# Kernel tuning notes

Measured on AMD Instinct MI355X. Metric: run time of the kernel, lower is better.

## Reference

```python
import jax, jax.numpy as jnp
import numpy as np

ALPHA = 0.7
MARGIN = 0.5
BATCH = 8192


def setup_inputs() -> dict:
    key = jax.random.key(0)
    k1, k2 = jax.random.split(key)
    predictions = jax.random.normal(k1, (BATCH, 1), dtype=jnp.float32)
    targets = jax.random.normal(k2, (BATCH, 1), dtype=jnp.float32)
    return {"predictions": predictions, "targets": targets}


def reference(predictions, targets):
    # MSE term (mean over all elements, as nn.MSELoss default)
    mse_loss = jnp.mean((predictions - targets) ** 2)

    p = predictions[:, 0]  # [B]
    t = targets[:, 0]      # [B]
    B = p.shape[0]

    # Pairwise differences [B, B]
    dt = t[:, None] - t[None, :]
    dp = p[:, None] - p[None, :]

    # Original loop visits ordered pairs i < j and, depending on sign(t_i - t_j),
    # computes relu(margin - sign(t_i - t_j) * (p_i - p_j)); ties are skipped.
    upper = jnp.triu(jnp.ones((B, B), dtype=bool), k=1)
    valid = upper & (dt != 0)
    pair_loss = jax.nn.relu(MARGIN - jnp.sign(dt) * dp)

    count = jnp.sum(valid)
    ranking_sum = jnp.sum(jnp.where(valid, pair_loss, 0.0))
    ranking_loss = jnp.where(count > 0, ranking_sum / jnp.maximum(count, 1), 0.0)

    return ALPHA * mse_loss + (1.0 - ALPHA) * ranking_loss
```

## Files before the change

### kernel.cpp

```cpp
#include <hip/hip_runtime.h>

#define ALPHA 0.7f
#define MARGIN 0.5f
#define TI 128
#define TJ 256

__global__ __launch_bounds__(256) void pair_kernel(const float* __restrict__ p,
                                                   const float* __restrict__ t,
                                                   int B,
                                                   float* __restrict__ bsum,
                                                   float* __restrict__ bmse,
                                                   int*   __restrict__ bcnt) {
    const int bid = blockIdx.x;
    int jt = (int)((sqrtf(4.0f * (float)bid + 1.0f) - 1.0f) * 0.5f);
    while ((jt + 1) * (jt + 2) <= bid) ++jt;
    while (jt * (jt + 1) > bid) --jt;
    const int it = bid - jt * (jt + 1);

    const int tid = threadIdx.x;
    const int ig0 = it * TI;
    const int jg  = jt * TJ + tid;

    __shared__ float s_t[TI];
    __shared__ float s_p[TI];
    if (tid < TI) {
        const int ig = ig0 + tid;
        const bool iv = ig < B;
        s_t[tid] = iv ? t[ig] : 0.0f;
        s_p[tid] = iv ? p[ig] : 0.0f;
    }
    __syncthreads();

    const bool jvalid = jg < B;
    const float tjv = jvalid ? t[jg] : 0.0f;
    const float pjv = jvalid ? p[jg] : 0.0f;

    float sum  = 0.0f;
    int   cnt  = 0;
    float msev = 0.0f;

    const bool fulltile = (ig0 + TI) <= jt * TJ;

    if (jvalid) {
        if (it == 2 * jt) {
            const float d = pjv - tjv;
            msev = d * d;
        }
        if (fulltile) {
            #pragma unroll 8
            for (int ii = 0; ii < TI; ++ii) {
                const float dt = s_t[ii] - tjv;
                const float dp = s_p[ii] - pjv;
                const float sdp = (dt > 0.0f) ? dp : -dp;
                const float v = fmaxf(MARGIN - sdp, 0.0f);
                const bool valid = (dt != 0.0f);
                sum += valid ? v : 0.0f;
                cnt += valid ? 1 : 0;
            }
        } else {
            const int ilim = min(TI, B - ig0);
            const int jloc = jg - ig0;
            #pragma unroll 4
            for (int ii = 0; ii < ilim; ++ii) {
                const float dt = s_t[ii] - tjv;
                const float dp = s_p[ii] - pjv;
                const float sdp = (dt > 0.0f) ? dp : -dp;
                const float v = fmaxf(MARGIN - sdp, 0.0f);
                const bool valid = (dt != 0.0f) && (ii < jloc);
                sum += valid ? v : 0.0f;
                cnt += valid ? 1 : 0;
            }
        }
    }

    for (int off = 32; off > 0; off >>= 1) {
        sum  += __shfl_down(sum, off);
        cnt  += __shfl_down(cnt, off);
        msev += __shfl_down(msev, off);
    }
    __shared__ float r_sum[4], r_mse[4];
    __shared__ int   r_cnt[4];
    const int wid  = tid >> 6;
    const int lane = tid & 63;
    if (lane == 0) { r_sum[wid] = sum; r_mse[wid] = msev; r_cnt[wid] = cnt; }
    __syncthreads();
    if (tid == 0) {
        bsum[bid] = r_sum[0] + r_sum[1] + r_sum[2] + r_sum[3];
        bmse[bid] = r_mse[0] + r_mse[1] + r_mse[2] + r_mse[3];
        bcnt[bid] = r_cnt[0] + r_cnt[1] + r_cnt[2] + r_cnt[3];
    }
}

__global__ __launch_bounds__(256) void finalize_kernel(const float* __restrict__ bsum,
                                                       const float* __restrict__ bmse,
                                                       const int*   __restrict__ bcnt,
                                                       int NB, int B,
                                                       float* __restrict__ out) {
    const int tid = threadIdx.x;
    double S = 0.0, M = 0.0;
    long long C = 0;
    for (int k = tid; k < NB; k += 256) {
        S += (double)bsum[k];
        M += (double)bmse[k];
        C += (long long)bcnt[k];
    }
    for (int off = 32; off > 0; off >>= 1) {
        S += __shfl_down(S, off);
        M += __shfl_down(M, off);
        C += __shfl_down(C, off);
    }
    __shared__ double rs[4], rm[4];
    __shared__ long long rc[4];
    const int wid  = tid >> 6;
    const int lane = tid & 63;
    if (lane == 0) { rs[wid] = S; rm[wid] = M; rc[wid] = C; }
    __syncthreads();
    if (tid == 0) {
        S = rs[0] + rs[1] + rs[2] + rs[3];
        M = rm[0] + rm[1] + rm[2] + rm[3];
        C = rc[0] + rc[1] + rc[2] + rc[3];
        const double mse  = M / (double)B;
        const double rank = (C > 0) ? (S / (double)(C > 1 ? C : 1)) : 0.0;
        out[0] = (float)((double)ALPHA * mse + (double)(1.0f - ALPHA) * rank);
    }
}

extern "C" void kernel_launch(void* const* d_in, const int* in_sizes, int n_in,
                              void* d_out, int out_size, void* d_ws, size_t ws_size,
                              hipStream_t stream) {
    const float* p = (const float*)d_in[0];
    const float* t = (const float*)d_in[1];
    const int B = in_sizes[0];

    const int NJ = (B + TJ - 1) / TJ;
    const int NB = NJ * (NJ + 1);

    float* bsum = (float*)d_ws;
    float* bmse = bsum + NB;
    int*   bcnt = (int*)(bmse + NB);

    pair_kernel<<<NB, TJ, 0, stream>>>(p, t, B, bsum, bmse, bcnt);
    finalize_kernel<<<1, 256, 0, stream>>>(bsum, bmse, bcnt, NB, B, (float*)d_out);
}
```

Baseline: 19.85 us.

## Register-block four j columns per thread with single-wave blocks and ballot counts

Each thread now handles four j columns in registers and loads them with float4 reads. Blocks shrink to one 64-lane wave, so the i-tile is 64 rows, and the triangular block mapping is redone for the finer tiles. Shared memory stores t and p as interleaved float2. The sign flip uses a bit XOR, and the valid-pair count uses ballot plus popcount instead of per-thread integer adds. The block-level shared reduction is dropped. The trade-off is more blocks, each with less work, and extra ballot instructions in the inner loop.

After: 22.50 us. 13.3% more time.

```diff
diff --git a/kernel.cpp b/kernel.cpp
--- a/kernel.cpp
+++ b/kernel.cpp
@@ -1,93 +1,119 @@
 #include <hip/hip_runtime.h>
 
-#define ALPHA 0.7f
+#define ALPHA  0.7f
 #define MARGIN 0.5f
-#define TI 128
+#define TI 64
 #define TJ 256
+#define JR 4
 
-__global__ __launch_bounds__(256) void pair_kernel(const float* __restrict__ p,
-                                                   const float* __restrict__ t,
-                                                   int B,
-                                                   float* __restrict__ bsum,
-                                                   float* __restrict__ bmse,
-                                                   int*   __restrict__ bcnt) {
+__global__ __launch_bounds__(64) void pair_kernel(const float* __restrict__ p,
+                                                  const float* __restrict__ t,
+                                                  int B,
+                                                  float* __restrict__ bsum,
+                                                  float* __restrict__ bmse,
+                                                  int*   __restrict__ bcnt) {
     const int bid = blockIdx.x;
-    int jt = (int)((sqrtf(4.0f * (float)bid + 1.0f) - 1.0f) * 0.5f);
-    while ((jt + 1) * (jt + 2) <= bid) ++jt;
-    while (jt * (jt + 1) > bid) --jt;
-    const int it = bid - jt * (jt + 1);
+    int jt = (int)((sqrtf(1.0f + 2.0f * (float)bid) - 1.0f) * 0.5f);
+    while (2 * (jt + 1) * (jt + 2) <= bid) ++jt;
+    while (2 * jt * (jt + 1) > bid) --jt;
+    const int it  = bid - 2 * jt * (jt + 1);
 
-    const int tid = threadIdx.x;
-    const int ig0 = it * TI;
-    const int jg  = jt * TJ + tid;
+    const int tid   = threadIdx.x;
+    const int ig0   = it * TI;
+    const int jbase = jt * TJ;
+    const int j0    = jbase + tid * JR;
 
-    __shared__ float s_t[TI];
-    __shared__ float s_p[TI];
-    if (tid < TI) {
+    __shared__ float2 s_tp[TI];
+    {
         const int ig = ig0 + tid;
-        const bool iv = ig < B;
-        s_t[tid] = iv ? t[ig] : 0.0f;
-        s_p[tid] = iv ? p[ig] : 0.0f;
+        float2 v;
+        if (ig < B) { v.x = t[ig]; v.y = p[ig]; }
+        else        { v.x = 0.0f;  v.y = 0.0f;  }
+        s_tp[tid] = v;
     }
     __syncthreads();
 
-    const bool jvalid = jg < B;
-    const float tjv = jvalid ? t[jg] : 0.0f;
-    const float pjv = jvalid ? p[jg] : 0.0f;
+    float tjv[JR], pjv[JR];
+    bool  jvb[JR];
+    if (j0 + JR <= B) {
+        const float4 tv = *reinterpret_cast<const float4*>(t + j0);
+        const float4 pv = *reinterpret_cast<const float4*>(p + j0);
+        tjv[0] = tv.x; tjv[1] = tv.y; tjv[2] = tv.z; tjv[3] = tv.w;
+        pjv[0] = pv.x; pjv[1] = pv.y; pjv[2] = pv.z; pjv[3] = pv.w;
+        jvb[0] = jvb[1] = jvb[2] = jvb[3] = true;
+    } else {
+        #pragma unroll
+        for (int k = 0; k < JR; ++k) {
+            const int jg = j0 + k;
+            jvb[k] = jg < B;
+            tjv[k] = jvb[k] ? t[jg] : 0.0f;
+            pjv[k] = jvb[k] ? p[jg] : 0.0f;
+        }
+    }
+    unsigned long long jm[JR];
+    #pragma unroll
+    for (int k = 0; k < JR; ++k) jm[k] = __ballot(jvb[k]);
 
-    float sum  = 0.0f;
-    int   cnt  = 0;
+    float sum[JR] = {0.0f, 0.0f, 0.0f, 0.0f};
+    int   cnt = 0;
     float msev = 0.0f;
 
-    const bool fulltile = (ig0 + TI) <= jt * TJ;
+    if (it == 4 * jt) {
+        #pragma unroll
+        for (int k = 0; k < JR; ++k) {
+            const float d = pjv[k] - tjv[k];
+            msev += jvb[k] ? d * d : 0.0f;
+        }
+    }
 
-    if (jvalid) {
-        if (it == 2 * jt) {
-            const float d = pjv - tjv;
-            msev = d * d;
+    if (it < 4 * jt) {
+        #pragma unroll 8
+        for (int ii = 0; ii < TI; ++ii) {
+            const float2 itp = s_tp[ii];
+            #pragma unroll
+            for (int k = 0; k < JR; ++k) {
+                const float dt = itp.x - tjv[k];
+                const float dp = itp.y - pjv[k];
+                const unsigned sg = __float_as_uint(dt) & 0x80000000u;
+                const float sdp = __uint_as_float(__float_as_uint(dp) ^ sg);
+                const float v = fmaxf(MARGIN - sdp, 0.0f);
+                const bool val = (dt != 0.0f);
+                sum[k] += val ? v : 0.0f;
+                cnt += (int)__popcll(__ballot(val) & jm[k]);
+            }
         }
-        if (fulltile) {
-            #pragma unroll 8
-            for (int ii = 0; ii < TI; ++ii) {
-                const float dt = s_t[ii] - tjv;
-                const float dp = s_p[ii] - pjv;
-                const float sdp = (dt > 0.0f) ? dp : -dp;
+    } else {
+        int jloc[JR];
+        #pragma unroll
+        for (int k = 0; k < JR; ++k) jloc[k] = j0 + k - ig0;
+        #pragma unroll 4
+        for (int ii = 0; ii < TI; ++ii) {
+            const float2 itp = s_tp[ii];
+            #pragma unroll
+            for (int k = 0; k < JR; ++k) {
+                const float dt = itp.x - tjv[k];
+                const float dp = itp.y - pjv[k];
+                const unsigned sg = __float_as_uint(dt) & 0x80000000u;
+                const float sdp = __uint_as_float(__float_as_uint(dp) ^ sg);
                 const float v = fmaxf(MARGIN - sdp, 0.0f);
-                const bool valid = (dt != 0.0f);
-                sum += valid ? v : 0.0f;
-                cnt += valid ? 1 : 0;
-            }
-        } else {
-            const int ilim = min(TI, B - ig0);
-            const int jloc = jg - ig0;
-            #pragma unroll 4
-            for (int ii = 0; ii < ilim; ++ii) {
-                const float dt = s_t[ii] - tjv;
-                const float dp = s_p[ii] - pjv;
-                const float sdp = (dt > 0.0f) ? dp : -dp;
-                const float v = fmaxf(MARGIN - sdp, 0.0f);
-                const bool valid = (dt != 0.0f) && (ii < jloc);
-                sum += valid ? v : 0.0f;
-                cnt += valid ? 1 : 0;
+                const bool val = (dt != 0.0f) && (ii < jloc[k]);
+                sum[k] += val ? v : 0.0f;
+                cnt += (int)__popcll(__ballot(val) & jm[k]);
             }
         }
     }
 
+    float stot = 0.0f;
+    #pragma unroll
+    for (int k = 0; k < JR; ++k) stot += jvb[k] ? sum[k] : 0.0f;
     for (int off = 32; off > 0; off >>= 1) {
-        sum  += __shfl_down(sum, off);
-        cnt  += __shfl_down(cnt, off);
+        stot += __shfl_down(stot, off);
         msev += __shfl_down(msev, off);
     }
-    __shared__ float r_sum[4], r_mse[4];
-    __shared__ int   r_cnt[4];
-    const int wid  = tid >> 6;
-    const int lane = tid & 63;
-    if (lane == 0) { r_sum[wid] = sum; r_mse[wid] = msev; r_cnt[wid] = cnt; }
-    __syncthreads();
     if (tid == 0) {
-        bsum[bid] = r_sum[0] + r_sum[1] + r_sum[2] + r_sum[3];
-        bmse[bid] = r_mse[0] + r_mse[1] + r_mse[2] + r_mse[3];
-        bcnt[bid] = r_cnt[0] + r_cnt[1] + r_cnt[2] + r_cnt[3];
+        bsum[bid] = stot;
+        bmse[bid] = msev;
+        bcnt[bid] = cnt;
     }
 }
 
@@ -111,8 +137,7 @@
     }
     __shared__ double rs[4], rm[4];
     __shared__ long long rc[4];
-    const int wid  = tid >> 6;
-    const int lane = tid & 63;
+    const int wid = tid >> 6, lane = tid & 63;
     if (lane == 0) { rs[wid] = S; rm[wid] = M; rc[wid] = C; }
     __syncthreads();
     if (tid == 0) {
@@ -133,12 +158,12 @@
     const int B = in_sizes[0];
 
     const int NJ = (B + TJ - 1) / TJ;
-    const int NB = NJ * (NJ + 1);
+    const int NB = 2 * NJ * (NJ + 1);
 
     float* bsum = (float*)d_ws;
     float* bmse = bsum + NB;
     int*   bcnt = (int*)(bmse + NB);
 
-    pair_kernel<<<NB, TJ, 0, stream>>>(p, t, B, bsum, bmse, bcnt);
+    pair_kernel<<<NB, 64, 0, stream>>>(p, t, B, bsum, bmse, bcnt);
     finalize_kernel<<<1, 256, 0, stream>>>(bsum, bmse, bcnt, NB, B, (float*)d_out);
 }
```

## Retile pair kernel with two j per thread and deferred tie handling

Applied to the files above, without the earlier changes.

Changes the tiling to 64-row i tiles by 512-column j tiles, with each thread handling two j elements loaded as float2. The i values now come straight from global memory as uniform loads instead of through shared memory. The sign flip becomes a bitwise XOR, and the tie check moves to a rare wave-uniform branch so the main loop is branch-free. The pair count is worked out in closed form minus the ties, and 4 blocks per SM are requested through launch bounds. The aim is fewer shared-memory and sync costs and more ILP per thread, at the price of more blocks and partials for the finalize kernel and reliance on scalar-cache hits for the i loads.

Measured after the change: 21.08 us. 6.2% more time.

```diff
diff --git a/kernel.cpp b/kernel.cpp
--- a/kernel.cpp
+++ b/kernel.cpp
@@ -1,93 +1,127 @@
 #include <hip/hip_runtime.h>
 
-#define ALPHA 0.7f
+#define ALPHA  0.7f
 #define MARGIN 0.5f
-#define TI 128
-#define TJ 256
+#define TI  64
+#define TJ  512
+#define JR  2
 
-__global__ __launch_bounds__(256) void pair_kernel(const float* __restrict__ p,
-                                                   const float* __restrict__ t,
-                                                   int B,
-                                                   float* __restrict__ bsum,
-                                                   float* __restrict__ bmse,
-                                                   int*   __restrict__ bcnt) {
+__global__ __launch_bounds__(256, 4)
+void pair_kernel(const float* __restrict__ p, const float* __restrict__ t,
+                 int B, float* __restrict__ bsum, float* __restrict__ bmse,
+                 int* __restrict__ bcnt) {
     const int bid = blockIdx.x;
-    int jt = (int)((sqrtf(4.0f * (float)bid + 1.0f) - 1.0f) * 0.5f);
-    while ((jt + 1) * (jt + 2) <= bid) ++jt;
-    while (jt * (jt + 1) > bid) --jt;
-    const int it = bid - jt * (jt + 1);
+    int jt = (int)((sqrtf((float)bid + 1.0f) - 1.0f) * 0.5f);
+    while (4 * (jt + 1) * (jt + 2) <= bid) ++jt;
+    while (4 * jt * (jt + 1) > bid) --jt;
+    const int it = bid - 4 * jt * (jt + 1);
 
-    const int tid = threadIdx.x;
-    const int ig0 = it * TI;
-    const int jg  = jt * TJ + tid;
+    const int tid   = threadIdx.x;
+    const int ibase = it * TI;
+    const int j0    = jt * TJ + tid * JR;
 
-    __shared__ float s_t[TI];
-    __shared__ float s_p[TI];
-    if (tid < TI) {
-        const int ig = ig0 + tid;
-        const bool iv = ig < B;
-        s_t[tid] = iv ? t[ig] : 0.0f;
-        s_p[tid] = iv ? p[ig] : 0.0f;
+    float tjv0, tjv1, pjv0, pjv1;
+    bool jv0, jv1;
+    if (j0 + JR <= B) {
+        const float2 tv = *reinterpret_cast<const float2*>(t + j0);
+        const float2 pv = *reinterpret_cast<const float2*>(p + j0);
+        tjv0 = tv.x; tjv1 = tv.y; pjv0 = pv.x; pjv1 = pv.y;
+        jv0 = jv1 = true;
+    } else {
+        jv0 = (j0 + 0) < B;
+        jv1 = (j0 + 1) < B;
+        tjv0 = jv0 ? t[j0]     : __int_as_float(0x7f800000);
+        tjv1 = jv1 ? t[j0 + 1] : __int_as_float(0x7f800000);
+        pjv0 = jv0 ? p[j0]     : 1e30f;
+        pjv1 = jv1 ? p[j0 + 1] : 1e30f;
     }
-    __syncthreads();
 
-    const bool jvalid = jg < B;
-    const float tjv = jvalid ? t[jg] : 0.0f;
-    const float pjv = jvalid ? p[jg] : 0.0f;
+    float sum = 0.0f, msev = 0.0f;
+    int   cnt = 0, tiec = 0;
 
-    float sum  = 0.0f;
-    int   cnt  = 0;
-    float msev = 0.0f;
+    if (it == 0) {
+        const float d0 = pjv0 - tjv0, d1 = pjv1 - tjv1;
+        msev += jv0 ? d0 * d0 : 0.0f;
+        msev += jv1 ? d1 * d1 : 0.0f;
+    }
 
-    const bool fulltile = (ig0 + TI) <= jt * TJ;
+    const int ilim = min(TI, B - ibase);
 
-    if (jvalid) {
-        if (it == 2 * jt) {
-            const float d = pjv - tjv;
-            msev = d * d;
-        }
-        if (fulltile) {
-            #pragma unroll 8
-            for (int ii = 0; ii < TI; ++ii) {
-                const float dt = s_t[ii] - tjv;
-                const float dp = s_p[ii] - pjv;
-                const float sdp = (dt > 0.0f) ? dp : -dp;
-                const float v = fmaxf(MARGIN - sdp, 0.0f);
-                const bool valid = (dt != 0.0f);
-                sum += valid ? v : 0.0f;
-                cnt += valid ? 1 : 0;
-            }
-        } else {
-            const int ilim = min(TI, B - ig0);
-            const int jloc = jg - ig0;
-            #pragma unroll 4
-            for (int ii = 0; ii < ilim; ++ii) {
-                const float dt = s_t[ii] - tjv;
-                const float dp = s_p[ii] - pjv;
-                const float sdp = (dt > 0.0f) ? dp : -dp;
-                const float v = fmaxf(MARGIN - sdp, 0.0f);
-                const bool valid = (dt != 0.0f) && (ii < jloc);
-                sum += valid ? v : 0.0f;
-                cnt += valid ? 1 : 0;
+    if (it < 8 * jt) {
+        #pragma unroll 8
+        for (int ii = 0; ii < TI; ++ii) {
+            const float ts = t[ibase + ii];
+            const float ps = p[ibase + ii];
+            const float dt0 = ts - tjv0;
+            const float dp0 = ps - pjv0;
+            const float sdp0 = __uint_as_float(__float_as_uint(dp0) ^
+                               (__float_as_uint(dt0) & 0x80000000u));
+            const float v0 = fmaxf(MARGIN - sdp0, 0.0f);
+            sum += v0;
+            const float dt1 = ts - tjv1;
+            const float dp1 = ps - pjv1;
+            const float sdp1 = __uint_as_float(__float_as_uint(dp1) ^
+                               (__float_as_uint(dt1) & 0x80000000u));
+            const float v1 = fmaxf(MARGIN - sdp1, 0.0f);
+            sum += v1;
+            const bool e0 = (dt0 == 0.0f);
+            const bool e1 = (dt1 == 0.0f);
+            if (__any(e0 || e1)) {
+                sum  -= e0 ? v0 : 0.0f;
+                sum  -= e1 ? v1 : 0.0f;
+                tiec += (e0 ? 1 : 0) + (e1 ? 1 : 0);
             }
         }
+        cnt += (jv0 ? TI : 0) + (jv1 ? TI : 0);
+    } else if (ilim > 0) {
+        const int jl0 = j0 - ibase;
+        const int jl1 = j0 + 1 - ibase;
+        #pragma unroll 4
+        for (int ii = 0; ii < ilim; ++ii) {
+            const float ts = t[ibase + ii];
+            const float ps = p[ibase + ii];
+            const bool in0 = ii < jl0;
+            const bool in1 = ii < jl1;
+            const float dt0 = ts - tjv0;
+            const float dp0 = ps - pjv0;
+            const float sdp0 = __uint_as_float(__float_as_uint(dp0) ^
+                               (__float_as_uint(dt0) & 0x80000000u));
+            const float v0 = fmaxf(MARGIN - sdp0, 0.0f);
+            sum += in0 ? v0 : 0.0f;
+            const float dt1 = ts - tjv1;
+            const float dp1 = ps - pjv1;
+            const float sdp1 = __uint_as_float(__float_as_uint(dp1) ^
+                               (__float_as_uint(dt1) & 0x80000000u));
+            const float v1 = fmaxf(MARGIN - sdp1, 0.0f);
+            sum += in1 ? v1 : 0.0f;
+            const bool e0 = (dt0 == 0.0f) && in0;
+            const bool e1 = (dt1 == 0.0f) && in1;
+            if (__any(e0 || e1)) {
+                sum  -= e0 ? v0 : 0.0f;
+                sum  -= e1 ? v1 : 0.0f;
+                tiec += (e0 ? 1 : 0) + (e1 ? 1 : 0);
+            }
+        }
+        int c0 = min(max(jl0, 0), ilim);
+        int c1 = min(max(jl1, 0), ilim);
+        cnt += (jv0 ? c0 : 0) + (jv1 ? c1 : 0);
     }
 
+    int cn = cnt - tiec;
     for (int off = 32; off > 0; off >>= 1) {
         sum  += __shfl_down(sum, off);
-        cnt  += __shfl_down(cnt, off);
         msev += __shfl_down(msev, off);
+        cn   += __shfl_down(cn, off);
     }
-    __shared__ float r_sum[4], r_mse[4];
-    __shared__ int   r_cnt[4];
-    const int wid  = tid >> 6;
-    const int lane = tid & 63;
-    if (lane == 0) { r_sum[wid] = sum; r_mse[wid] = msev; r_cnt[wid] = cnt; }
+    __shared__ float rs[4], rm[4];
+    __shared__ int   rc[4];
+    const int wid = tid >> 6, lane = tid & 63;
+    if (lane == 0) { rs[wid] = sum; rm[wid] = msev; rc[wid] = cn; }
     __syncthreads();
     if (tid == 0) {
-        bsum[bid] = r_sum[0] + r_sum[1] + r_sum[2] + r_sum[3];
-        bmse[bid] = r_mse[0] + r_mse[1] + r_mse[2] + r_mse[3];
-        bcnt[bid] = r_cnt[0] + r_cnt[1] + r_cnt[2] + r_cnt[3];
+        bsum[bid] = rs[0] + rs[1] + rs[2] + rs[3];
+        bmse[bid] = rm[0] + rm[1] + rm[2] + rm[3];
+        bcnt[bid] = rc[0] + rc[1] + rc[2] + rc[3];
     }
 }
 
@@ -111,8 +145,7 @@
     }
     __shared__ double rs[4], rm[4];
     __shared__ long long rc[4];
-    const int wid  = tid >> 6;
-    const int lane = tid & 63;
+    const int wid = tid >> 6, lane = tid & 63;
     if (lane == 0) { rs[wid] = S; rm[wid] = M; rc[wid] = C; }
     __syncthreads();
     if (tid == 0) {
@@ -133,12 +166,12 @@
     const int B = in_sizes[0];
 
     const int NJ = (B + TJ - 1) / TJ;
-    const int NB = NJ * (NJ + 1);
+    const int NB = 4 * NJ * (NJ + 1);
 
     float* bsum = (float*)d_ws;
     float* bmse = bsum + NB;
     int*   bcnt = (int*)(bmse + NB);
 
-    pair_kernel<<<NB, TJ, 0, stream>>>(p, t, B, bsum, bmse, bcnt);
+    pair_kernel<<<NB, 256, 0, stream>>>(p, t, B, bsum, bmse, bcnt);
     finalize_kernel<<<1, 256, 0, stream>>>(bsum, bmse, bcnt, NB, B, (float*)d_out);
 }
```
